# Kernel tuning notes

Hardware: AMD Instinct MI355X
Metric: run time of the kernel (lower is better)

The kernel has to match this reference:

```python
import jax, jax.numpy as jnp
import numpy as np

TEMP = 0.3  # softmax temperature used in load-balance loss


def setup_inputs() -> dict:
    key = jax.random.key(0)
    k1, k2 = jax.random.split(key)
    num_tokens, d_model, num_expert = 16384, 4096, 128
    inp = jax.random.normal(k1, (num_tokens, d_model), dtype=jnp.float32)
    wg = jax.random.normal(k2, (num_expert, d_model), dtype=jnp.float32) * (1.0 / np.sqrt(d_model))
    return {"inp": inp, "wg": wg, "top_k": 2}


def reference(inp, wg, top_k):
    # Gate logits: [T, E] = [T, D] @ [D, E]
    logits = jnp.einsum("td,ed->te", inp, wg)
    # Top-k selection + softmax over the k selected logits
    top_vals, top_idx = jax.lax.top_k(logits, top_k)  # [T, k]
    gate_score = jax.nn.softmax(top_vals, axis=-1)    # [T, k]
    # Load-balance loss (stored as self.loss in torch; returned here)
    T, E = logits.shape
    probs = jax.nn.softmax(logits / TEMP, axis=-1)    # [T, E]
    mask = jax.nn.one_hot(top_idx[:, 0], E, dtype=probs.dtype) * (E / T)
    me = jnp.sum(probs, axis=0)                       # [E]
    ce = jnp.sum(mask, axis=0)                        # [E]
    loss = jnp.sum(me * ce) / T
    return top_idx, gate_score, loss
```

## Files before the change

### kernel.cpp

```cpp
#include <hip/hip_runtime.h>

typedef _Float16 half8 __attribute__((ext_vector_type(8)));
typedef float floatx4 __attribute__((ext_vector_type(4)));

#define NTOK 16384
#define DM   4096
#define NE   128
#define MT   32
#define BK   64
#define KSPLIT 2
#define KHALF (DM / KSPLIT)
#define NITER (KHALF / BK)
#define NBLK_MAIN (NTOK / MT * KSPLIT)
#define ET   64
#define NBLK_EPI (NTOK / ET)
#define TEMP 0.3f
#define CSTRIDE 528
#define ABUF (8 * CSTRIDE)
#define BUFSZ (2 * ABUF)

__global__ void pack_b_kernel(const float* __restrict__ wg, _Float16* __restrict__ Bp) {
    int gtid = blockIdx.x * blockDim.x + threadIdx.x;
    int l  = gtid & 63;
    int tg = gtid >> 6;
    int g  = tg & 7;
    int kc = tg >> 3;
    const float* src = wg + (size_t)(g * 16 + (l & 15)) * DM + kc * 32 + (l >> 4) * 8;
    float4 v0 = *(const float4*)src;
    float4 v1 = *(const float4*)(src + 4);
    float f[8] = {v0.x, v0.y, v0.z, v0.w, v1.x, v1.y, v1.z, v1.w};
    half8 h1, h2;
#pragma unroll
    for (int j = 0; j < 8; j++) {
        h1[j] = (_Float16)f[j];
        h2[j] = (_Float16)((f[j] - (float)h1[j]) * 2048.0f);
    }
    char* dst = (char*)Bp + (size_t)tg * 2048 + l * 16;
    *(half8*)dst = h1;
    *(half8*)(dst + 1024) = h2;
}

__device__ __forceinline__ void stage_write(unsigned char* base, unsigned off,
                                            float4 v0, float4 v1) {
    float f[8] = {v0.x, v0.y, v0.z, v0.w, v1.x, v1.y, v1.z, v1.w};
    half8 h1, h2;
#pragma unroll
    for (int j = 0; j < 8; j++) {
        h1[j] = (_Float16)f[j];
        h2[j] = (_Float16)((f[j] - (float)h1[j]) * 2048.0f);
    }
    *(half8*)(base + off) = h1;
    *(half8*)(base + ABUF + off) = h2;
}

__launch_bounds__(256, 4)
__global__ void moe_gemm_kernel(const float* __restrict__ A,
                                const _Float16* __restrict__ Bp,
                                float* __restrict__ part) {
    __shared__ __align__(16) unsigned char smem[2 * BUFSZ];
    const int tid  = threadIdx.x;
    const int wave = tid >> 6;
    const int lane = tid & 63;
    const int quad = lane >> 4;
    const int lrow = lane & 15;
    const int half = blockIdx.x & 1;
    const int tok0 = (blockIdx.x >> 1) * MT;

    const int srow = tid >> 3;
    const int schunk = tid & 7;
    const float* aptr = A + (size_t)(tok0 + srow) * DM + half * KHALF + schunk * 8;
    const unsigned swoff = schunk * CSTRIDE + srow * 16;
    const unsigned aroff = quad * CSTRIDE + lrow * 16;

    const char* bB = (const char*)Bp + (size_t)half * (1u << 20) + (wave * 2) * 2048 + lane * 16;

    floatx4 accm[2][2], accc[2][2];
#pragma unroll
    for (int r = 0; r < 2; r++)
#pragma unroll
        for (int c = 0; c < 2; c++) {
            accm[r][c] = (floatx4){0.f, 0.f, 0.f, 0.f};
            accc[r][c] = (floatx4){0.f, 0.f, 0.f, 0.f};
        }

    {
        float4 v0 = *(const float4*)aptr;
        float4 v1 = *(const float4*)(aptr + 4);
        stage_write(smem, swoff, v0, v1);
    }
    __syncthreads();

    for (int it = 0; it < NITER; ++it) {
        float4 n0, n1;
        if (it < NITER - 1) {
            const float* p = aptr + (it + 1) * BK;
            n0 = *(const float4*)p;
            n1 = *(const float4*)(p + 4);
        }
        unsigned char* cb = smem + (it & 1) * BUFSZ;
        const char* bit = bB + (size_t)it * 32768;

#pragma unroll
        for (int ks = 0; ks < 2; ++ks) {
            half8 b1f[2], b2f[2], a1[2], a2[2];
#pragma unroll
            for (int c = 0; c < 2; c++) {
                b1f[c] = *(const half8*)(bit + ks * 16384 + c * 2048);
                b2f[c] = *(const half8*)(bit + ks * 16384 + c * 2048 + 1024);
            }
#pragma unroll
            for (int r = 0; r < 2; r++) {
                a1[r] = *(const half8*)(cb + ks * 2112 + r * 256 + aroff);
                a2[r] = *(const half8*)(cb + ABUF + ks * 2112 + r * 256 + aroff);
            }
#pragma unroll
            for (int r = 0; r < 2; r++)
#pragma unroll
                for (int c = 0; c < 2; c++) {
                    accm[r][c] = __builtin_amdgcn_mfma_f32_16x16x32_f16(a1[r], b1f[c], accm[r][c], 0, 0, 0);
                    accc[r][c] = __builtin_amdgcn_mfma_f32_16x16x32_f16(a1[r], b2f[c], accc[r][c], 0, 0, 0);
                    accc[r][c] = __builtin_amdgcn_mfma_f32_16x16x32_f16(a2[r], b1f[c], accc[r][c], 0, 0, 0);
                }
        }
        if (it < NITER - 1)
            stage_write(smem + ((it + 1) & 1) * BUFSZ, swoff, n0, n1);
        __syncthreads();
    }

    float* pbase = part + (size_t)half * NTOK * NE;
#pragma unroll
    for (int r = 0; r < 2; r++)
#pragma unroll
        for (int c = 0; c < 2; c++) {
            floatx4 v;
#pragma unroll
            for (int g = 0; g < 4; g++)
                v[g] = accm[r][c][g] + accc[r][c][g] * (1.0f / 2048.0f);
            int e = wave * 32 + c * 16 + lrow;
            int t = tok0 + r * 16 + quad * 4;
            *(floatx4*)(pbase + (size_t)e * NTOK + t) = v;
        }
}

__global__ void topk_kernel(const float* __restrict__ part,
                            float* __restrict__ out,
                            float* __restrict__ me_part,
                            float* __restrict__ ce_part) {
    __shared__ float LG[NE * 68];
    __shared__ float tmax[ET], tscale[ET];
    __shared__ int hist[NE];
    const int tid = threadIdx.x;
    const int t0  = blockIdx.x * ET;
    const float* p0 = part;
    const float* p1 = part + (size_t)NTOK * NE;

    {
        const int q = tid & 3;
#pragma unroll
        for (int pass = 0; pass < 2; pass++) {
            int e = (tid >> 2) + pass * 64;
            const float* r0 = p0 + (size_t)e * NTOK + t0 + q * 16;
            const float* r1 = p1 + (size_t)e * NTOK + t0 + q * 16;
            float* dst = LG + e * 68 + q * 16;
#pragma unroll
            for (int j = 0; j < 16; j += 4) {
                float4 a = *(const float4*)(r0 + j);
                float4 b = *(const float4*)(r1 + j);
                float4 s = {a.x + b.x, a.y + b.y, a.z + b.z, a.w + b.w};
                *(float4*)(dst + j) = s;
            }
        }
    }
    if (tid < NE) hist[tid] = 0;
    __syncthreads();

    if (tid < ET) {
        const int t = tid;
        float m1 = -1e30f, m2 = -1e30f;
        int i1 = 0, i2 = 0;
        for (int e = 0; e < NE; e++) {
            float v = LG[e * 68 + t];
            if (v > m1) { m2 = m1; i2 = i1; m1 = v; i1 = e; }
            else if (v > m2) { m2 = v; i2 = e; }
        }
        float s = 0.f;
        for (int e = 0; e < NE; e++)
            s += __expf((LG[e * 68 + t] - m1) * (1.0f / TEMP));
        tmax[t] = m1;
        tscale[t] = 1.0f / s;
        atomicAdd(&hist[i1], 1);

        const int tg = t0 + t;
        out[tg * 2 + 0] = (float)i1;
        out[tg * 2 + 1] = (float)i2;
        float d = __expf(m2 - m1);
        float g1 = 1.0f / (1.0f + d);
        out[2 * NTOK + tg * 2 + 0] = g1;
        out[2 * NTOK + tg * 2 + 1] = d * g1;
    }
    __syncthreads();

    if (tid < NE) {
        const int e = tid;
        float s = 0.f;
        for (int t = 0; t < ET; t++)
            s += __expf((LG[e * 68 + t] - tmax[t]) * (1.0f / TEMP)) * tscale[t];
        me_part[blockIdx.x * NE + e] = s;
        ce_part[blockIdx.x * NE + e] = (float)hist[e];
    }
}

__global__ void finalize_kernel(const float* __restrict__ mp, const float* __restrict__ cp,
                                float* __restrict__ out) {
    __shared__ float red[2 * 8 * 128];
    __shared__ float wsum[2];
    const int tid = threadIdx.x;
    const int e = tid & 127, seg = tid >> 7;
    float sm = 0.f, sc = 0.f;
    for (int b = seg; b < NBLK_EPI; b += 8) {
        sm += mp[b * NE + e];
        sc += cp[b * NE + e];
    }
    red[seg * 128 + e] = sm;
    red[1024 + seg * 128 + e] = sc;
    __syncthreads();
    if (tid < 128) {
        float me = 0.f, ce = 0.f;
#pragma unroll
        for (int s = 0; s < 8; s++) {
            me += red[s * 128 + tid];
            ce += red[1024 + s * 128 + tid];
        }
        ce *= (float)NE / (float)NTOK;
        float v = me * ce;
#pragma unroll
        for (int off = 32; off; off >>= 1) v += __shfl_down(v, off);
        if ((tid & 63) == 0) wsum[tid >> 6] = v;
    }
    __syncthreads();
    if (tid == 0) out[4 * NTOK] = (wsum[0] + wsum[1]) / (float)NTOK;
}

extern "C" void kernel_launch(void* const* d_in, const int* in_sizes, int n_in,
                              void* d_out, int out_size, void* d_ws, size_t ws_size,
                              hipStream_t stream) {
    (void)in_sizes; (void)n_in; (void)out_size; (void)ws_size;
    const float* inp = (const float*)d_in[0];
    const float* wg  = (const float*)d_in[1];
    float* out = (float*)d_out;

    _Float16* Bp = (_Float16*)d_ws;
    float* part = (float*)((char*)d_ws + (2u << 20));
    float* mp = (float*)((char*)d_ws + (18u << 20));
    float* cp = mp + NBLK_EPI * NE;

    pack_b_kernel<<<256, 256, 0, stream>>>(wg, Bp);
    moe_gemm_kernel<<<NBLK_MAIN, 256, 0, stream>>>(inp, Bp, part);
    topk_kernel<<<NBLK_EPI, 256, 0, stream>>>(part, out, mp, cp);
    finalize_kernel<<<1, 1024, 0, stream>>>(mp, cp, out);
}
```

Before: 426.8 us.

## Load A directly into MFMA registers, dropping shared-memory staging and barriers

Each wave now loads its own A fragments straight from global memory in MFMA layout and does the fp16 hi/lo split in registers, so the LDS double buffer and per-iteration __syncthreads are gone. This is meant to remove LDS write/read traffic and barrier stalls. In exchange, all four waves now load the same A rows (4x redundant global/L2 traffic), and the loads are no longer prefetched one iteration ahead, so memory latency may be exposed.

New measurement: 511.4 us. +19.8%, slower.

```diff
diff --git a/kernel.cpp b/kernel.cpp
--- a/kernel.cpp
+++ b/kernel.cpp
@@ -15,9 +15,6 @@
 #define ET   64
 #define NBLK_EPI (NTOK / ET)
 #define TEMP 0.3f
-#define CSTRIDE 528
-#define ABUF (8 * CSTRIDE)
-#define BUFSZ (2 * ABUF)
 
 __global__ void pack_b_kernel(const float* __restrict__ wg, _Float16* __restrict__ Bp) {
     int gtid = blockIdx.x * blockDim.x + threadIdx.x;
@@ -40,39 +37,21 @@
     *(half8*)(dst + 1024) = h2;
 }
 
-__device__ __forceinline__ void stage_write(unsigned char* base, unsigned off,
-                                            float4 v0, float4 v1) {
-    float f[8] = {v0.x, v0.y, v0.z, v0.w, v1.x, v1.y, v1.z, v1.w};
-    half8 h1, h2;
-#pragma unroll
-    for (int j = 0; j < 8; j++) {
-        h1[j] = (_Float16)f[j];
-        h2[j] = (_Float16)((f[j] - (float)h1[j]) * 2048.0f);
-    }
-    *(half8*)(base + off) = h1;
-    *(half8*)(base + ABUF + off) = h2;
-}
-
 __launch_bounds__(256, 4)
 __global__ void moe_gemm_kernel(const float* __restrict__ A,
                                 const _Float16* __restrict__ Bp,
                                 float* __restrict__ part) {
-    __shared__ __align__(16) unsigned char smem[2 * BUFSZ];
     const int tid  = threadIdx.x;
     const int wave = tid >> 6;
     const int lane = tid & 63;
     const int quad = lane >> 4;
     const int lrow = lane & 15;
-    const int half = blockIdx.x & 1;
+    const int hf   = blockIdx.x & 1;
     const int tok0 = (blockIdx.x >> 1) * MT;
 
-    const int srow = tid >> 3;
-    const int schunk = tid & 7;
-    const float* aptr = A + (size_t)(tok0 + srow) * DM + half * KHALF + schunk * 8;
-    const unsigned swoff = schunk * CSTRIDE + srow * 16;
-    const unsigned aroff = quad * CSTRIDE + lrow * 16;
-
-    const char* bB = (const char*)Bp + (size_t)half * (1u << 20) + (wave * 2) * 2048 + lane * 16;
+    const float* ar0 = A + (size_t)(tok0 + lrow) * DM + hf * KHALF + quad * 8;
+    const float* ar1 = ar0 + (size_t)16 * DM;
+    const char* bB = (const char*)Bp + (size_t)hf * (1u << 20) + (wave * 2) * 2048 + lane * 16;
 
     floatx4 accm[2][2], accc[2][2];
 #pragma unroll
@@ -83,35 +62,38 @@
             accc[r][c] = (floatx4){0.f, 0.f, 0.f, 0.f};
         }
 
-    {
-        float4 v0 = *(const float4*)aptr;
-        float4 v1 = *(const float4*)(aptr + 4);
-        stage_write(smem, swoff, v0, v1);
-    }
-    __syncthreads();
-
     for (int it = 0; it < NITER; ++it) {
-        float4 n0, n1;
-        if (it < NITER - 1) {
-            const float* p = aptr + (it + 1) * BK;
-            n0 = *(const float4*)p;
-            n1 = *(const float4*)(p + 4);
-        }
-        unsigned char* cb = smem + (it & 1) * BUFSZ;
+        const int kbase = it * BK;
+        float4 av[2][2][2];
+#pragma unroll
+        for (int r = 0; r < 2; r++) {
+            const float* ar = r ? ar1 : ar0;
+#pragma unroll
+            for (int ks = 0; ks < 2; ks++) {
+                av[r][ks][0] = *(const float4*)(ar + kbase + ks * 32);
+                av[r][ks][1] = *(const float4*)(ar + kbase + ks * 32 + 4);
+            }
+        }
         const char* bit = bB + (size_t)it * 32768;
 
 #pragma unroll
         for (int ks = 0; ks < 2; ++ks) {
-            half8 b1f[2], b2f[2], a1[2], a2[2];
+            half8 b1f[2], b2f[2];
 #pragma unroll
             for (int c = 0; c < 2; c++) {
                 b1f[c] = *(const half8*)(bit + ks * 16384 + c * 2048);
                 b2f[c] = *(const half8*)(bit + ks * 16384 + c * 2048 + 1024);
             }
+            half8 a1[2], a2[2];
 #pragma unroll
             for (int r = 0; r < 2; r++) {
-                a1[r] = *(const half8*)(cb + ks * 2112 + r * 256 + aroff);
-                a2[r] = *(const half8*)(cb + ABUF + ks * 2112 + r * 256 + aroff);
+                float f[8] = {av[r][ks][0].x, av[r][ks][0].y, av[r][ks][0].z, av[r][ks][0].w,
+                              av[r][ks][1].x, av[r][ks][1].y, av[r][ks][1].z, av[r][ks][1].w};
+#pragma unroll
+                for (int j = 0; j < 8; j++) {
+                    a1[r][j] = (_Float16)f[j];
+                    a2[r][j] = (_Float16)((f[j] - (float)a1[r][j]) * 2048.0f);
+                }
             }
 #pragma unroll
             for (int r = 0; r < 2; r++)
@@ -122,12 +104,9 @@
                     accc[r][c] = __builtin_amdgcn_mfma_f32_16x16x32_f16(a2[r], b1f[c], accc[r][c], 0, 0, 0);
                 }
         }
-        if (it < NITER - 1)
-            stage_write(smem + ((it + 1) & 1) * BUFSZ, swoff, n0, n1);
-        __syncthreads();
-    }
-
-    float* pbase = part + (size_t)half * NTOK * NE;
+    }
+
+    float* pbase = part + (size_t)hf * NTOK * NE;
 #pragma unroll
     for (int r = 0; r < 2; r++)
 #pragma unroll
```
